# Kernel optimization log

Measured on AMD Instinct MI355X. Metric: run time of the kernel, lower is better.

## Reference

```python
import jax, jax.numpy as jnp
import numpy as np

B, C, H, W = 4, 256, 48, 48
NH = 4                 # num_heads
HD = C // NH           # head_dim = 64
KD = HD // 2           # key_dim = 32 (attn_ratio=0.5)
QKV_C = C + 2 * KD * NH  # 512
FF = 2 * C             # 512
EPS = 1e-3             # ultralytics BatchNorm2d eps


def _bn(x, g, b, m, v):
    # eval-mode BatchNorm2d over channel dim 1 of NCHW
    s = g / jnp.sqrt(v + EPS)
    return x * s[:, None, None] + (b - m * s)[:, None, None]


def _conv1x1(x, w):
    # w: [out_c, in_c]
    return jnp.einsum('bchw,oc->bohw', x, w)


def _dwconv3x3(x, w):
    # depthwise 3x3, padding 1; w: [C, 1, 3, 3]
    return jax.lax.conv_general_dilated(
        x, w, (1, 1), [(1, 1), (1, 1)],
        dimension_numbers=('NCHW', 'OIHW', 'NCHW'),
        feature_group_count=C)


def setup_inputs() -> dict:
    key = jax.random.key(0)
    ks = jax.random.split(key, 32)
    d = {}
    d['x'] = jax.random.normal(ks[0], (B, C, H, W), dtype=jnp.float32)

    def bn_params(i, ch):
        g = 0.5 + jax.random.uniform(ks[i], (ch,), dtype=jnp.float32)
        b = 0.1 * jax.random.normal(ks[i + 1], (ch,), dtype=jnp.float32)
        m = 0.1 * jax.random.normal(ks[i + 2], (ch,), dtype=jnp.float32)
        v = 0.5 + jax.random.uniform(ks[i + 3], (ch,), dtype=jnp.float32)
        return g, b, m, v

    d['qkv_w'] = 0.05 * jax.random.normal(ks[1], (QKV_C, C), dtype=jnp.float32)
    d['qkv_g'], d['qkv_b'], d['qkv_m'], d['qkv_v'] = bn_params(2, QKV_C)
    d['pe_w'] = 0.1 * jax.random.normal(ks[6], (C, 1, 3, 3), dtype=jnp.float32)
    d['pe_g'], d['pe_b'], d['pe_m'], d['pe_v'] = bn_params(7, C)
    d['proj_w'] = 0.05 * jax.random.normal(ks[11], (C, C), dtype=jnp.float32)
    d['proj_g'], d['proj_b'], d['proj_m'], d['proj_v'] = bn_params(12, C)
    d['f1_w'] = 0.05 * jax.random.normal(ks[16], (FF, C), dtype=jnp.float32)
    d['f1_g'], d['f1_b'], d['f1_m'], d['f1_v'] = bn_params(17, FF)
    d['f2_w'] = 0.05 * jax.random.normal(ks[21], (C, FF), dtype=jnp.float32)
    d['f2_g'], d['f2_b'], d['f2_m'], d['f2_v'] = bn_params(22, C)
    return d


def reference(x, qkv_w, qkv_g, qkv_b, qkv_m, qkv_v,
              pe_w, pe_g, pe_b, pe_m, pe_v,
              proj_w, proj_g, proj_b, proj_m, proj_v,
              f1_w, f1_g, f1_b, f1_m, f1_v,
              f2_w, f2_g, f2_b, f2_m, f2_v):
    b, c, h, w = x.shape
    n = h * w
    # --- Attention ---
    qkv = _bn(_conv1x1(x, qkv_w), qkv_g, qkv_b, qkv_m, qkv_v)
    qkv = qkv.reshape(b, NH, 2 * KD + HD, n)
    q = qkv[:, :, :KD]            # [b, nh, kd, n]
    k = qkv[:, :, KD:2 * KD]      # [b, nh, kd, n]
    v = qkv[:, :, 2 * KD:]        # [b, nh, hd, n]
    attn = jnp.einsum('bhkn,bhkm->bhnm', q, k) * (KD ** -0.5)
    attn = jax.nn.softmax(attn, axis=-1)
    o = jnp.einsum('bhdm,bhnm->bhdn', v, attn).reshape(b, c, h, w)
    pe = _bn(_dwconv3x3(v.reshape(b, c, h, w), pe_w), pe_g, pe_b, pe_m, pe_v)
    attn_out = _bn(_conv1x1(o + pe, proj_w), proj_g, proj_b, proj_m, proj_v)
    x = x + attn_out  # shortcut
    # --- FFN ---
    f = _conv1x1(x, f1_w)
    f = _bn(f, f1_g, f1_b, f1_m, f1_v)
    f = f * jax.nn.sigmoid(f)  # SiLU
    f = _bn(_conv1x1(f, f2_w), f2_g, f2_b, f2_m, f2_v)
    return x + f  # shortcut
```

## Files before the change

### kernel.cpp

```cpp
#include <hip/hip_runtime.h>
#include <math.h>

#define Bb   4
#define Cc   256
#define Hh   48
#define Ww   48
#define NNp  2304
#define Rr   9216
#define NHd  4
#define QKVC 512
#define EPSf 1e-3f

typedef unsigned int   u32;
typedef unsigned short u16;
typedef __attribute__((ext_vector_type(8))) __bf16 bf16x8;
typedef __attribute__((ext_vector_type(4))) float  f32x4;

#if __has_builtin(__builtin_amdgcn_exp2f)
#define EXP2F(x) __builtin_amdgcn_exp2f(x)
#else
#define EXP2F(x) __expf((x) * 0.6931471805599453f)
#endif

__device__ __forceinline__ u16 f2bf(float f) {
    u32 u = __float_as_uint(f);
    u = (u + 0x7fffu + ((u >> 16) & 1u)) >> 16;
    return (u16)u;
}
__device__ __forceinline__ float bf2f(u16 h) {
    return __uint_as_float((u32)h << 16);
}
__device__ __forceinline__ u32 pk2bf(float a, float b) {
    union { __bf16 h; u16 u; } ua, ub;
    ua.h = (__bf16)a; ub.h = (__bf16)b;
    return (u32)ua.u | ((u32)ub.u << 16);
}
__device__ __forceinline__ void gload16(const void* gsrc, void* ldst) {
    __builtin_amdgcn_global_load_lds(
        (const __attribute__((address_space(1))) u32*)gsrc,
        (__attribute__((address_space(3))) u32*)ldst, 16, 0, 0);
}

__global__ __launch_bounds__(256)
void prep_fused(const float* __restrict__ W0, const float* __restrict__ g0, const float* __restrict__ b0, const float* __restrict__ m0, const float* __restrict__ v0, u16* __restrict__ Wb0, float* __restrict__ bi0,
                const float* __restrict__ W1, const float* __restrict__ g1, const float* __restrict__ b1, const float* __restrict__ m1, const float* __restrict__ v1, u16* __restrict__ Wb1, float* __restrict__ bi1,
                const float* __restrict__ W2, const float* __restrict__ g2, const float* __restrict__ b2, const float* __restrict__ m2, const float* __restrict__ v2, u16* __restrict__ Wb2, float* __restrict__ bi2,
                const float* __restrict__ W3, const float* __restrict__ g3, const float* __restrict__ b3, const float* __restrict__ m3, const float* __restrict__ v3, u16* __restrict__ Wb3, float* __restrict__ bi3,
                const float* __restrict__ x, u16* __restrict__ Xt)
{
    const int bid = blockIdx.x;
    const int tid = threadIdx.x;
    if (bid < 384) {
        const int row = bid * 4 + (tid >> 6);
        const int lane = tid & 63;
        const float *W, *gp, *bp, *mp, *vp;
        u16* Wb; float* bias;
        int K = 256, oc;
        float c = 1.f;
        if (row < 512) {
            oc = row; W = W0; gp = g0; bp = b0; mp = m0; vp = v0; Wb = Wb0; bias = bi0;
            if ((oc & 127) < 32) c = 0.17677669529663687f * 1.4426950408889634f;
        } else if (row < 768) {
            oc = row - 512; W = W1; gp = g1; bp = b1; mp = m1; vp = v1; Wb = Wb1; bias = bi1;
        } else if (row < 1280) {
            oc = row - 768; W = W2; gp = g2; bp = b2; mp = m2; vp = v2; Wb = Wb2; bias = bi2;
        } else {
            oc = row - 1280; W = W3; gp = g3; bp = b3; mp = m3; vp = v3; Wb = Wb3; bias = bi3;
            K = 512;
        }
        const float s = gp[oc] * rsqrtf(vp[oc] + EPSf);
        if (lane == 0) bias[oc] = (bp[oc] - mp[oc] * s) * c;
        const float sc = s * c;
        for (int k0 = lane * 4; k0 < K; k0 += 256) {
            const float4 w = *(const float4*)(W + (size_t)oc * K + k0);
            u32 lo = (u32)f2bf(w.x * sc) | ((u32)f2bf(w.y * sc) << 16);
            u32 hi = (u32)f2bf(w.z * sc) | ((u32)f2bf(w.w * sc) << 16);
            *(uint2*)(Wb + (size_t)oc * K + k0) = make_uint2(lo, hi);
        }
        return;
    }
    const int cb = bid - 384;
    const int b  = cb / 144;
    const int rm = cb - b * 144;
    const int c0 = (rm / 36) * 64;
    const int n0 = (rm % 36) * 64;
    __shared__ float tile[64][65];
    {
        const int n = tid & 63, cl = tid >> 6;
        #pragma unroll
        for (int cc = 0; cc < 16; ++cc) {
            const int c = cc * 4 + cl;
            tile[c][n] = x[((size_t)b * Cc + c0 + c) * NNp + n0 + n];
        }
    }
    __syncthreads();
    {
        const int n = tid >> 2, q = tid & 3;
        #pragma unroll
        for (int j = 0; j < 2; ++j) {
            const int ch = q * 2 + j, c = ch * 8;
            u32 w[4];
            #pragma unroll
            for (int e = 0; e < 4; ++e)
                w[e] = (u32)f2bf(tile[c + 2*e][n]) | ((u32)f2bf(tile[c + 2*e + 1][n]) << 16);
            *(uint4*)(Xt + ((size_t)b * NNp + n0 + n) * Cc + c0 + c)
                = make_uint4(w[0], w[1], w[2], w[3]);
        }
    }
}

template<int MODE>
__global__ __launch_bounds__(256)
void gemm64(const u16* __restrict__ A, const u16* __restrict__ Bx,
            const float* __restrict__ bias, const float* __restrict__ resid,
            float* __restrict__ Yf, u16* __restrict__ Yt, int M, int K)
{
    const int r0 = blockIdx.x * 64;
    const int m0 = blockIdx.y * 64;
    const int tid = threadIdx.x;
    const int lane = tid & 63, wid = tid >> 6;
    const int g = lane >> 4, i16 = lane & 15;

    __shared__ __align__(16) u16 Al[2][4][64][8];
    __shared__ __align__(16) u16 Bl[2][4][64][8];

    f32x4 acc[4];
    #pragma unroll
    for (int j = 0; j < 4; ++j) acc[j] = (f32x4){0.f, 0.f, 0.f, 0.f};

    gload16(A + (size_t)(m0 + (tid & 63)) * K + (tid >> 6) * 8,
            (u16*)&Al[0][0][0][0] + (size_t)tid * 8);
    gload16(Bx + (size_t)(r0 + (tid & 63)) * K + (tid >> 6) * 8,
            (u16*)&Bl[0][0][0][0] + (size_t)tid * 8);
    __syncthreads();

    int buf = 0;
    for (int k0 = 0; k0 < K; k0 += 32) {
        if (k0 + 32 < K) {
            const int kn = k0 + 32;
            gload16(A + (size_t)(m0 + (tid & 63)) * K + kn + (tid >> 6) * 8,
                    (u16*)&Al[buf ^ 1][0][0][0] + (size_t)tid * 8);
            gload16(Bx + (size_t)(r0 + (tid & 63)) * K + kn + (tid >> 6) * 8,
                    (u16*)&Bl[buf ^ 1][0][0][0] + (size_t)tid * 8);
        }
        const bf16x8 af = *(const bf16x8*)&Al[buf][g][wid * 16 + i16][0];
        bf16x8 bf[4];
        #pragma unroll
        for (int bo = 0; bo < 4; ++bo)
            bf[bo] = *(const bf16x8*)&Bl[buf][g][bo * 16 + i16][0];
        __builtin_amdgcn_s_setprio(1);
        #pragma unroll
        for (int bo = 0; bo < 4; ++bo)
            acc[bo] = __builtin_amdgcn_mfma_f32_16x16x32_bf16(af, bf[bo], acc[bo], 0, 0, 0);
        __builtin_amdgcn_s_setprio(0);
        __syncthreads();
        buf ^= 1;
    }

    const int b  = r0 / NNp;
    const int nb = r0 - b * NNp;
    const int oc0 = m0 + wid * 16 + g * 4;
    const float4 t4 = *(const float4*)(bias + oc0);
    #pragma unroll
    for (int bo = 0; bo < 4; ++bo) {
        const int nloc = bo * 16 + i16;
        float y[4];
        y[0] = acc[bo][0] + t4.x;  y[1] = acc[bo][1] + t4.y;
        y[2] = acc[bo][2] + t4.z;  y[3] = acc[bo][3] + t4.w;
        if (MODE == 1 || MODE == 3) {
            const int n = nb + nloc;
            const size_t base = ((size_t)b * M + oc0) * NNp + n;
            #pragma unroll
            for (int r = 0; r < 4; ++r) {
                y[r] += resid[base + (size_t)r * NNp];
                Yf[base + (size_t)r * NNp] = y[r];
            }
        }
        if (MODE == 2) {
            #pragma unroll
            for (int r = 0; r < 4; ++r) y[r] = y[r] / (1.f + __expf(-y[r]));
        }
        if (MODE != 3) {
            const size_t rG = (size_t)(r0 + nloc);
            *(uint2*)(Yt + rG * M + oc0) = make_uint2(pk2bf(y[0], y[1]), pk2bf(y[2], y[3]));
        }
    }
}

__global__ __launch_bounds__(256)
void repack_v(const u16* __restrict__ Yt, u16* __restrict__ Vb)
{
    const int m0 = blockIdx.x * 64;
    const int h = blockIdx.y, b = blockIdx.z;
    const int bh = b * NHd + h;
    __shared__ u16 vt[64][72];
    const int tid = threadIdx.x;
    #pragma unroll
    for (int ii = 0; ii < 2; ++ii) {
        const int mm = ii * 32 + (tid >> 3);
        const int ch = tid & 7;
        *(uint4*)&vt[mm][ch * 8] =
            *(const uint4*)(Yt + ((size_t)b * NNp + m0 + mm) * QKVC + h * 128 + 64 + ch * 8);
    }
    __syncthreads();
    const int d = tid >> 2, mq = tid & 3;
    #pragma unroll
    for (int j = 0; j < 2; ++j) {
        const int mc = mq * 2 + j;
        u32 w[4];
        #pragma unroll
        for (int e = 0; e < 4; ++e)
            w[e] = (u32)vt[mc * 8 + 2*e][d] | ((u32)vt[mc * 8 + 2*e + 1][d] << 16);
        *(uint4*)(Vb + ((size_t)bh * 64 + d) * NNp + m0 + mc * 8)
            = make_uint4(w[0], w[1], w[2], w[3]);
    }
}

__global__ __launch_bounds__(256)
void pe_pre(const u16* __restrict__ Yt, const float* __restrict__ pw,
            const float* __restrict__ gg, const float* __restrict__ bb,
            const float* __restrict__ mm, const float* __restrict__ vv,
            u16* __restrict__ PEb)
{
    const int tid = threadIdx.x;
    const int h = blockIdx.y, b = blockIdx.z;
    const int p = blockIdx.x * 32 + (tid >> 3);
    const int ch = tid & 7;
    const int c0 = h * 64 + ch * 8;
    const int yy = p / Ww, xx = p - yy * Ww;

    float acc[8];
    #pragma unroll
    for (int j = 0; j < 8; ++j) acc[j] = 0.f;

    #pragma unroll
    for (int dy = -1; dy <= 1; ++dy) {
        const int Y = yy + dy;
        if (Y < 0 || Y >= Hh) continue;
        #pragma unroll
        for (int dx = -1; dx <= 1; ++dx) {
            const int X = xx + dx;
            if (X < 0 || X >= Ww) continue;
            const uint4 raw = *(const uint4*)(Yt +
                ((size_t)b * NNp + Y * Ww + X) * QKVC + h * 128 + 64 + ch * 8);
            const u32* rw = (const u32*)&raw;
            #pragma unroll
            for (int j = 0; j < 8; ++j) {
                const u16 hv = (u16)(rw[j >> 1] >> (16 * (j & 1)));
                acc[j] += pw[(size_t)(c0 + j) * 9 + (dy + 1) * 3 + (dx + 1)] * bf2f(hv);
            }
        }
    }

    u32 res[4];
    #pragma unroll
    for (int e = 0; e < 4; ++e) {
        const int j0 = 2 * e, j1 = 2 * e + 1;
        const float s0 = gg[c0 + j0] * rsqrtf(vv[c0 + j0] + EPSf);
        const float s1 = gg[c0 + j1] * rsqrtf(vv[c0 + j1] + EPSf);
        res[e] = pk2bf(acc[j0] * s0 + (bb[c0 + j0] - mm[c0 + j0] * s0),
                       acc[j1] * s1 + (bb[c0 + j1] - mm[c0 + j1] * s1));
    }
    *(uint4*)(PEb + ((size_t)b * NNp + p) * Cc + c0) = make_uint4(res[0], res[1], res[2], res[3]);
}

__global__ __launch_bounds__(128)
void attn_mfma(const u16* __restrict__ Yt, const u16* __restrict__ Vb,
               const u16* __restrict__ PEb, u16* __restrict__ Ot)
{
    __shared__ __align__(16) u16 Klds[2][4][64][8];
    __shared__ __align__(16) u16 Vlds[2][64][8][8];
    __shared__ __align__(16) u32 Plds[2][16][36];

    const int tid  = threadIdx.x;
    const int wid  = tid >> 6;
    const int lane = tid & 63;
    const int g    = lane >> 4;
    const int i16  = lane & 15;

    const int wg  = blockIdx.x;
    const int swz = (wg & 7) * 144 + (wg >> 3);
    const int xq  = swz % 72;
    const int bh  = swz / 72;
    const int h   = bh & 3, b = bh >> 2;

    const size_t bG = (size_t)b * NNp;
    const u16* Vg = Vb + (size_t)bh * 64 * NNp;

    const int nq = xq * 32 + wid * 16 + i16;
    const bf16x8 qfrag = *(const bf16x8*)(Yt + (bG + nq) * QKVC + h * 128 + g * 8);

    bf16x8 ones;
    { uint4 ov = make_uint4(0x3f803f80u, 0x3f803f80u, 0x3f803f80u, 0x3f803f80u);
      ones = *(bf16x8*)&ov; }

    const f32x4 zero = {0.f, 0.f, 0.f, 0.f};
    f32x4 oacc[4];
    f32x4 lacc = zero;
    #pragma unroll
    for (int d = 0; d < 4; ++d) oacc[d] = zero;
    float m_run = -1e30f;

    #pragma unroll
    for (int ii = 0; ii < 2; ++ii) {
        const int ci = ii * 128 + tid;
        gload16(Yt + (bG + (ci & 63)) * QKVC + h * 128 + 32 + (ci >> 6) * 8,
                (u16*)&Klds[0][0][0][0] + (size_t)ci * 8);
    }
    #pragma unroll
    for (int ii = 0; ii < 4; ++ii) {
        const int idx = ii * 128 + tid;
        const int d = idx >> 3, cp = idx & 7;
        gload16(Vg + (size_t)d * NNp + (cp ^ (d & 7)) * 8,
                (u16*)&Vlds[0][0][0][0] + (size_t)idx * 8);
    }
    __syncthreads();

    int cur = 0;
    for (int t = 0; t < 36; ++t) {
        if (t < 35) {
            const int m0 = (t + 1) * 64;
            #pragma unroll
            for (int ii = 0; ii < 2; ++ii) {
                const int ci = ii * 128 + tid;
                gload16(Yt + (bG + m0 + (ci & 63)) * QKVC + h * 128 + 32 + (ci >> 6) * 8,
                        (u16*)&Klds[cur ^ 1][0][0][0] + (size_t)ci * 8);
            }
            #pragma unroll
            for (int ii = 0; ii < 4; ++ii) {
                const int idx = ii * 128 + tid;
                const int d = idx >> 3, cp = idx & 7;
                gload16(Vg + (size_t)d * NNp + m0 + (cp ^ (d & 7)) * 8,
                        (u16*)&Vlds[cur ^ 1][0][0][0] + (size_t)idx * 8);
            }
        }

        f32x4 sac[4];
        __builtin_amdgcn_s_setprio(1);
        #pragma unroll
        for (int j = 0; j < 4; ++j) {
            const bf16x8 kf = *(const bf16x8*)&Klds[cur][g][16 * j + i16][0];
            sac[j] = __builtin_amdgcn_mfma_f32_16x16x32_bf16(kf, qfrag, zero, 0, 0, 0);
        }
        __builtin_amdgcn_s_setprio(0);

        float pm = sac[0][0];
        #pragma unroll
        for (int j = 0; j < 4; ++j)
            #pragma unroll
            for (int r = 0; r < 4; ++r) pm = fmaxf(pm, sac[j][r]);
        pm = fmaxf(pm, __shfl_xor(pm, 16));
        pm = fmaxf(pm, __shfl_xor(pm, 32));

        if (!__all(pm <= m_run + 8.f)) {
            const float mn = fmaxf(m_run, pm);
            const float fc = EXP2F(m_run - mn);
            m_run = mn;
            lacc[0] *= fc; lacc[1] *= fc; lacc[2] *= fc; lacc[3] *= fc;
            #pragma unroll
            for (int d = 0; d < 4; ++d) {
                oacc[d][0] *= fc; oacc[d][1] *= fc;
                oacc[d][2] *= fc; oacc[d][3] *= fc;
            }
        }

        {
            u32* prow = &Plds[wid][i16][0];
            #pragma unroll
            for (int j = 0; j < 4; ++j) {
                const float p0 = EXP2F(sac[j][0] - m_run);
                const float p1 = EXP2F(sac[j][1] - m_run);
                const float p2 = EXP2F(sac[j][2] - m_run);
                const float p3 = EXP2F(sac[j][3] - m_run);
                *(uint2*)&prow[8 * j + 2 * g] = make_uint2(pk2bf(p0, p1), pk2bf(p2, p3));
            }
        }

        const int d7 = i16 & 7;
        __builtin_amdgcn_s_setprio(1);
        #pragma unroll
        for (int s = 0; s < 2; ++s) {
            const bf16x8 pf = *(const bf16x8*)&Plds[wid][i16][16 * s + 4 * g];
            lacc = __builtin_amdgcn_mfma_f32_16x16x32_bf16(ones, pf, lacc, 0, 0, 0);
            #pragma unroll
            for (int db = 0; db < 4; ++db) {
                const bf16x8 vf = *(const bf16x8*)&Vlds[cur][db * 16 + i16][(4 * s + g) ^ d7][0];
                oacc[db] = __builtin_amdgcn_mfma_f32_16x16x32_bf16(vf, pf, oacc[db], 0, 0, 0);
            }
        }
        __builtin_amdgcn_s_setprio(0);

        __syncthreads();
        cur ^= 1;
    }

    const float linv = 1.f / lacc[0];
    const u16* pb = PEb + (bG + nq) * Cc + h * 64;
    u16* ob = Ot + (bG + nq) * Cc + h * 64;
    #pragma unroll
    for (int db = 0; db < 4; ++db) {
        const uint2 pv = *(const uint2*)(pb + db * 16 + g * 4);
        const float y0 = oacc[db][0] * linv + bf2f((u16)(pv.x & 0xffff));
        const float y1 = oacc[db][1] * linv + bf2f((u16)(pv.x >> 16));
        const float y2 = oacc[db][2] * linv + bf2f((u16)(pv.y & 0xffff));
        const float y3 = oacc[db][3] * linv + bf2f((u16)(pv.y >> 16));
        *(uint2*)(ob + db * 16 + g * 4) = make_uint2(pk2bf(y0, y1), pk2bf(y2, y3));
    }
}

extern "C" void kernel_launch(void* const* d_in, const int* in_sizes, int n_in,
                              void* d_out, int out_size, void* d_ws, size_t ws_size,
                              hipStream_t stream)
{
    const float* x      = (const float*)d_in[0];
    const float* qkv_w  = (const float*)d_in[1];
    const float* qkv_g  = (const float*)d_in[2];
    const float* qkv_b  = (const float*)d_in[3];
    const float* qkv_m  = (const float*)d_in[4];
    const float* qkv_v  = (const float*)d_in[5];
    const float* pe_w   = (const float*)d_in[6];
    const float* pe_g   = (const float*)d_in[7];
    const float* pe_b   = (const float*)d_in[8];
    const float* pe_m   = (const float*)d_in[9];
    const float* pe_v   = (const float*)d_in[10];
    const float* proj_w = (const float*)d_in[11];
    const float* proj_g = (const float*)d_in[12];
    const float* proj_b = (const float*)d_in[13];
    const float* proj_m = (const float*)d_in[14];
    const float* proj_v = (const float*)d_in[15];
    const float* f1_w   = (const float*)d_in[16];
    const float* f1_g   = (const float*)d_in[17];
    const float* f1_b   = (const float*)d_in[18];
    const float* f1_m   = (const float*)d_in[19];
    const float* f1_v   = (const float*)d_in[20];
    const float* f2_w   = (const float*)d_in[21];
    const float* f2_g   = (const float*)d_in[22];
    const float* f2_b   = (const float*)d_in[23];
    const float* f2_m   = (const float*)d_in[24];
    const float* f2_v   = (const float*)d_in[25];

    char* wsb = (char*)d_ws;
    u16*   Yt   = (u16*)(wsb);
    u16*   Xt   = (u16*)(wsb + 9437184);
    u16*   Vb   = (u16*)(wsb + 14155776);
    u16*   Ot   = (u16*)(wsb + 18874368);
    float* x1f  = (float*)(wsb + 23592960);
    u16*   PEb  = (u16*)(wsb + 23592960);
    u16*   Wq   = (u16*)(wsb + 33030144);
    u16*   Wp   = (u16*)(wsb + 33292288);
    u16*   W1   = (u16*)(wsb + 33423360);
    u16*   W2   = (u16*)(wsb + 33685504);
    float* biq  = (float*)(wsb + 33947648);
    float* bip  = (float*)(wsb + 33949696);
    float* bi1  = (float*)(wsb + 33950720);
    float* bi2  = (float*)(wsb + 33952768);
    u16*   Ft   = Yt;
    u16*   X1t  = Xt;
    float* out  = (float*)d_out;

    prep_fused<<<dim3(960), dim3(256), 0, stream>>>(
        qkv_w, qkv_g, qkv_b, qkv_m, qkv_v, Wq, biq,
        proj_w, proj_g, proj_b, proj_m, proj_v, Wp, bip,
        f1_w, f1_g, f1_b, f1_m, f1_v, W1, bi1,
        f2_w, f2_g, f2_b, f2_m, f2_v, W2, bi2,
        x, Xt);

    gemm64<0><<<dim3(144, 8), dim3(256), 0, stream>>>(
        Wq, Xt, biq, nullptr, nullptr, Yt, QKVC, 256);

    repack_v<<<dim3(36, 4, 4), dim3(256), 0, stream>>>(Yt, Vb);
    pe_pre<<<dim3(72, 4, 4), dim3(256), 0, stream>>>(Yt, pe_w, pe_g, pe_b, pe_m, pe_v, PEb);
    attn_mfma<<<dim3(1152), dim3(128), 0, stream>>>(Yt, Vb, PEb, Ot);

    gemm64<1><<<dim3(144, 4), dim3(256), 0, stream>>>(
        Wp, Ot, bip, x, x1f, X1t, Cc, 256);

    gemm64<2><<<dim3(144, 8), dim3(256), 0, stream>>>(
        W1, X1t, bi1, nullptr, nullptr, Ft, QKVC, 256);

    gemm64<3><<<dim3(144, 4), dim3(256), 0, stream>>>(
        W2, Ft, bi2, x1f, out, nullptr, Cc, 512);
}
```

Before: 145.3 us.

## Split attention over two key halves and merge partial softmax results

The attention kernel now splits each query tile's key range into two halves, doubling the grid from 1152 to 2304 workgroups. A new merge kernel combines the two partial outputs by rescaling with their running max and sum, then adds the positional-encoding term. The V repack and the positional-encoding kernels are also fused into a single launch that writes PE directly into the output buffer. The aim is better occupancy on the many-CU GPU and fewer launches, at the cost of writing and re-reading the bf16 partial outputs plus an extra kernel launch.

```diff
diff --git a/kernel.cpp b/kernel.cpp
--- a/kernel.cpp
+++ b/kernel.cpp
@@ -188,43 +188,45 @@
 }
 
 __global__ __launch_bounds__(256)
-void repack_v(const u16* __restrict__ Yt, u16* __restrict__ Vb)
+void vprep(const u16* __restrict__ Yt, u16* __restrict__ Vb,
+           const float* __restrict__ pw,
+           const float* __restrict__ gg, const float* __restrict__ bb,
+           const float* __restrict__ mm, const float* __restrict__ vv,
+           u16* __restrict__ PEb)
 {
-    const int m0 = blockIdx.x * 64;
-    const int h = blockIdx.y, b = blockIdx.z;
-    const int bh = b * NHd + h;
-    __shared__ u16 vt[64][72];
+    const int bid = blockIdx.x;
     const int tid = threadIdx.x;
-    #pragma unroll
-    for (int ii = 0; ii < 2; ++ii) {
-        const int mm = ii * 32 + (tid >> 3);
-        const int ch = tid & 7;
-        *(uint4*)&vt[mm][ch * 8] =
-            *(const uint4*)(Yt + ((size_t)b * NNp + m0 + mm) * QKVC + h * 128 + 64 + ch * 8);
-    }
-    __syncthreads();
-    const int d = tid >> 2, mq = tid & 3;
-    #pragma unroll
-    for (int j = 0; j < 2; ++j) {
-        const int mc = mq * 2 + j;
-        u32 w[4];
-        #pragma unroll
-        for (int e = 0; e < 4; ++e)
-            w[e] = (u32)vt[mc * 8 + 2*e][d] | ((u32)vt[mc * 8 + 2*e + 1][d] << 16);
-        *(uint4*)(Vb + ((size_t)bh * 64 + d) * NNp + m0 + mc * 8)
-            = make_uint4(w[0], w[1], w[2], w[3]);
-    }
-}
-
-__global__ __launch_bounds__(256)
-void pe_pre(const u16* __restrict__ Yt, const float* __restrict__ pw,
-            const float* __restrict__ gg, const float* __restrict__ bb,
-            const float* __restrict__ mm, const float* __restrict__ vv,
-            u16* __restrict__ PEb)
-{
-    const int tid = threadIdx.x;
-    const int h = blockIdx.y, b = blockIdx.z;
-    const int p = blockIdx.x * 32 + (tid >> 3);
+    if (bid < 576) {
+        const int m0 = (bid % 36) * 64;
+        const int h  = (bid / 36) & 3;
+        const int b  = bid / 144;
+        const int bh = b * NHd + h;
+        __shared__ u16 vt[64][72];
+        #pragma unroll
+        for (int ii = 0; ii < 2; ++ii) {
+            const int mmr = ii * 32 + (tid >> 3);
+            const int ch = tid & 7;
+            *(uint4*)&vt[mmr][ch * 8] =
+                *(const uint4*)(Yt + ((size_t)b * NNp + m0 + mmr) * QKVC + h * 128 + 64 + ch * 8);
+        }
+        __syncthreads();
+        const int d = tid >> 2, mq = tid & 3;
+        #pragma unroll
+        for (int j = 0; j < 2; ++j) {
+            const int mc = mq * 2 + j;
+            u32 w[4];
+            #pragma unroll
+            for (int e = 0; e < 4; ++e)
+                w[e] = (u32)vt[mc * 8 + 2*e][d] | ((u32)vt[mc * 8 + 2*e + 1][d] << 16);
+            *(uint4*)(Vb + ((size_t)bh * 64 + d) * NNp + m0 + mc * 8)
+                = make_uint4(w[0], w[1], w[2], w[3]);
+        }
+        return;
+    }
+    const int pid = bid - 576;
+    const int p  = (pid % 72) * 32 + (tid >> 3);
+    const int h  = (pid / 72) & 3;
+    const int b  = pid / 288;
     const int ch = tid & 7;
     const int c0 = h * 64 + ch * 8;
     const int yy = p / Ww, xx = p - yy * Ww;
@@ -266,7 +268,7 @@
 
 __global__ __launch_bounds__(128)
 void attn_mfma(const u16* __restrict__ Yt, const u16* __restrict__ Vb,
-               const u16* __restrict__ PEb, u16* __restrict__ Ot)
+               u16* __restrict__ PartO, float* __restrict__ Pml)
 {
     __shared__ __align__(16) u16 Klds[2][4][64][8];
     __shared__ __align__(16) u16 Vlds[2][64][8][8];
@@ -279,9 +281,11 @@
     const int i16  = lane & 15;
 
     const int wg  = blockIdx.x;
-    const int swz = (wg & 7) * 144 + (wg >> 3);
-    const int xq  = swz % 72;
-    const int bh  = swz / 72;
+    const int idx = (wg & 7) * 288 + (wg >> 3);
+    const int kh  = idx & 1;
+    const int qt  = idx >> 1;
+    const int xq  = qt % 72;
+    const int bh  = qt / 72;
     const int h   = bh & 3, b = bh >> 2;
 
     const size_t bG = (size_t)b * NNp;
@@ -301,37 +305,40 @@
     for (int d = 0; d < 4; ++d) oacc[d] = zero;
     float m_run = -1e30f;
 
+    const int t0 = kh * 18;
+
     #pragma unroll
     for (int ii = 0; ii < 2; ++ii) {
         const int ci = ii * 128 + tid;
-        gload16(Yt + (bG + (ci & 63)) * QKVC + h * 128 + 32 + (ci >> 6) * 8,
+        gload16(Yt + (bG + t0 * 64 + (ci & 63)) * QKVC + h * 128 + 32 + (ci >> 6) * 8,
                 (u16*)&Klds[0][0][0][0] + (size_t)ci * 8);
     }
     #pragma unroll
     for (int ii = 0; ii < 4; ++ii) {
-        const int idx = ii * 128 + tid;
-        const int d = idx >> 3, cp = idx & 7;
-        gload16(Vg + (size_t)d * NNp + (cp ^ (d & 7)) * 8,
-                (u16*)&Vlds[0][0][0][0] + (size_t)idx * 8);
+        const int idx2 = ii * 128 + tid;
+        const int d = idx2 >> 3, cp = idx2 & 7;
+        gload16(Vg + (size_t)d * NNp + t0 * 64 + (cp ^ (d & 7)) * 8,
+                (u16*)&Vlds[0][0][0][0] + (size_t)idx2 * 8);
     }
     __syncthreads();
 
     int cur = 0;
-    for (int t = 0; t < 36; ++t) {
-        if (t < 35) {
-            const int m0 = (t + 1) * 64;
+    for (int t = 0; t < 18; ++t) {
+        const int m0k = (t0 + t) * 64;
+        if (t < 17) {
+            const int mn = m0k + 64;
             #pragma unroll
             for (int ii = 0; ii < 2; ++ii) {
                 const int ci = ii * 128 + tid;
-                gload16(Yt + (bG + m0 + (ci & 63)) * QKVC + h * 128 + 32 + (ci >> 6) * 8,
+                gload16(Yt + (bG + mn + (ci & 63)) * QKVC + h * 128 + 32 + (ci >> 6) * 8,
                         (u16*)&Klds[cur ^ 1][0][0][0] + (size_t)ci * 8);
             }
             #pragma unroll
             for (int ii = 0; ii < 4; ++ii) {
-                const int idx = ii * 128 + tid;
-                const int d = idx >> 3, cp = idx & 7;
-                gload16(Vg + (size_t)d * NNp + m0 + (cp ^ (d & 7)) * 8,
-                        (u16*)&Vlds[cur ^ 1][0][0][0] + (size_t)idx * 8);
+                const int idx2 = ii * 128 + tid;
+                const int d = idx2 >> 3, cp = idx2 & 7;
+                gload16(Vg + (size_t)d * NNp + mn + (cp ^ (d & 7)) * 8,
+                        (u16*)&Vlds[cur ^ 1][0][0][0] + (size_t)idx2 * 8);
             }
         }
 
@@ -394,18 +401,59 @@
         cur ^= 1;
     }
 
-    const float linv = 1.f / lacc[0];
-    const u16* pb = PEb + (bG + nq) * Cc + h * 64;
-    u16* ob = Ot + (bG + nq) * Cc + h * 64;
+    const int qloc = wid * 16 + i16;
+    const int prow = (qt * 2 + kh) * 32 + qloc;
+    if (g == 0) {
+        Pml[(size_t)prow * 2 + 0] = m_run;
+        Pml[(size_t)prow * 2 + 1] = lacc[0];
+    }
+    u16* po = PartO + (size_t)prow * 64;
     #pragma unroll
     for (int db = 0; db < 4; ++db) {
-        const uint2 pv = *(const uint2*)(pb + db * 16 + g * 4);
-        const float y0 = oacc[db][0] * linv + bf2f((u16)(pv.x & 0xffff));
-        const float y1 = oacc[db][1] * linv + bf2f((u16)(pv.x >> 16));
-        const float y2 = oacc[db][2] * linv + bf2f((u16)(pv.y & 0xffff));
-        const float y3 = oacc[db][3] * linv + bf2f((u16)(pv.y >> 16));
-        *(uint2*)(ob + db * 16 + g * 4) = make_uint2(pk2bf(y0, y1), pk2bf(y2, y3));
-    }
+        *(uint2*)(po + db * 16 + g * 4) =
+            make_uint2(pk2bf(oacc[db][0], oacc[db][1]), pk2bf(oacc[db][2], oacc[db][3]));
+    }
+}
+
+__global__ __launch_bounds__(256)
+void merge_attn(const u16* __restrict__ PartO, const float* __restrict__ Pml,
+                u16* __restrict__ Ot)
+{
+    const int gid = blockIdx.x * 256 + threadIdx.x;
+    const int row = gid >> 3;
+    const int ch  = gid & 7;
+    const int qt  = row >> 5;
+    const int q   = row & 31;
+    const int bh  = qt / 72;
+    const int xq  = qt - bh * 72;
+    const int h   = bh & 3, b = bh >> 2;
+
+    const int p0 = (qt * 2) * 32 + q;
+    const int p1 = p0 + 32;
+    const float2 ml0 = *(const float2*)(Pml + (size_t)p0 * 2);
+    const float2 ml1 = *(const float2*)(Pml + (size_t)p1 * 2);
+    const float m  = fmaxf(ml0.x, ml1.x);
+    const float fa = EXP2F(ml0.x - m);
+    const float fb = EXP2F(ml1.x - m);
+    const float inv = 1.f / (ml0.y * fa + ml1.y * fb);
+
+    const uint4 a4 = *(const uint4*)(PartO + (size_t)p0 * 64 + ch * 8);
+    const uint4 b4 = *(const uint4*)(PartO + (size_t)p1 * 64 + ch * 8);
+    u16* dst = Ot + ((size_t)b * NNp + xq * 32 + q) * Cc + h * 64 + ch * 8;
+    const uint4 pe4 = *(const uint4*)dst;
+    const u32* aw = (const u32*)&a4;
+    const u32* bw = (const u32*)&b4;
+    const u32* pw = (const u32*)&pe4;
+    u32 res[4];
+    #pragma unroll
+    for (int e = 0; e < 4; ++e) {
+        const float y0 = (bf2f((u16)(aw[e] & 0xffff)) * fa + bf2f((u16)(bw[e] & 0xffff)) * fb) * inv
+                       + bf2f((u16)(pw[e] & 0xffff));
+        const float y1 = (bf2f((u16)(aw[e] >> 16))    * fa + bf2f((u16)(bw[e] >> 16))    * fb) * inv
+                       + bf2f((u16)(pw[e] >> 16));
+        res[e] = pk2bf(y0, y1);
+    }
+    *(uint4*)dst = make_uint4(res[0], res[1], res[2], res[3]);
 }
 
 extern "C" void kernel_launch(void* const* d_in, const int* in_sizes, int n_in,
@@ -445,7 +493,6 @@
     u16*   Vb   = (u16*)(wsb + 14155776);
     u16*   Ot   = (u16*)(wsb + 18874368);
     float* x1f  = (float*)(wsb + 23592960);
-    u16*   PEb  = (u16*)(wsb + 23592960);
     u16*   Wq   = (u16*)(wsb + 33030144);
     u16*   Wp   = (u16*)(wsb + 33292288);
     u16*   W1   = (u16*)(wsb + 33423360);
@@ -456,6 +503,8 @@
     float* bi2  = (float*)(wsb + 33952768);
     u16*   Ft   = Yt;
     u16*   X1t  = Xt;
+    float* Pml  = (float*)Xt;
+    u16*   PartO= (u16*)x1f;
     float* out  = (float*)d_out;
 
     prep_fused<<<dim3(960), dim3(256), 0, stream>>>(
@@ -468,9 +517,11 @@
     gemm64<0><<<dim3(144, 8), dim3(256), 0, stream>>>(
         Wq, Xt, biq, nullptr, nullptr, Yt, QKVC, 256);
 
-    repack_v<<<dim3(36, 4, 4), dim3(256), 0, stream>>>(Yt, Vb);
-    pe_pre<<<dim3(72, 4, 4), dim3(256), 0, stream>>>(Yt, pe_w, pe_g, pe_b, pe_m, pe_v, PEb);
-    attn_mfma<<<dim3(1152), dim3(128), 0, stream>>>(Yt, Vb, PEb, Ot);
+    vprep<<<dim3(1728), dim3(256), 0, stream>>>(
+        Yt, Vb, pe_w, pe_g, pe_b, pe_m, pe_v, Ot);
+
+    attn_mfma<<<dim3(2304), dim3(128), 0, stream>>>(Yt, Vb, PartO, Pml);
+    merge_attn<<<dim3(1152), dim3(256), 0, stream>>>(PartO, Pml, Ot);
 
     gemm64<1><<<dim3(144, 4), dim3(256), 0, stream>>>(
         Wp, Ot, bip, x, x1f, X1t, Cc, 256);
```

After: 146.3 us. No clear change (+0.7%).
